# Performance work log

Hardware: AMD Instinct MI355X
Metric: run time of the kernel (lower is better)

## Reference

```python
import jax, jax.numpy as jnp
import numpy as np

ALPHA = 0.2  # LeakyReLU negative slope
N = 1024     # num_particles
DIM = 3
F_IN = 2 * DIM   # 6
NH = 64          # n_hidden_features
H = 4            # n_heads
T = 12


def _gat_attend(feat, a_vec, slope):
    # feat: (..., N, K); a_vec: (..., 2K) split into source/dest halves
    k = feat.shape[-1]
    f_src = jnp.einsum('...nk,...k->...n', feat, a_vec[..., :k])
    f_dst = jnp.einsum('...nk,...k->...n', feat, a_vec[..., k:])
    e = jax.nn.leaky_relu(f_src[..., :, None] + f_dst[..., None, :], slope)
    attn = jax.nn.softmax(e, axis=-1)  # (..., N, N) dense particle attention
    return jnp.einsum('...ij,...jk->...ik', attn, feat)


def pat_layer(x, W_heads, a_heads, W_out, a_out):
    # x: (N, F_IN); W_heads: (H, F_IN, NH); a_heads: (H, 2*NH)
    # W_out: (H*NH, F_OUT); a_out: (2*F_OUT)
    hW = jnp.einsum('nf,hfk->hnk', x, W_heads)          # (H, N, NH)
    heads = jax.nn.elu(_gat_attend(hW, a_heads, ALPHA))  # (H, N, NH)
    x2 = heads.transpose(1, 0, 2).reshape(x.shape[0], -1)  # (N, H*NH) concat
    hW2 = x2 @ W_out                                     # (N, F_OUT)
    return _gat_attend(hW2, a_out, ALPHA)                # output head, no elu


def setup_inputs() -> dict:
    key = jax.random.key(0)
    ks = jax.random.split(key, 13)
    s = 0.1
    d = {'states': jax.random.normal(ks[0], (T, N, F_IN), jnp.float32)}
    names = ['Wx', 'ax', 'Wxo', 'axo', 'Wh', 'ah', 'Who', 'aho', 'Wy', 'ay', 'Wyo', 'ayo']
    shapes = [(H, F_IN, NH), (H, 2 * NH), (H * NH, F_IN), (2 * F_IN)] * 3
    for i, (nm, sh) in enumerate(zip(names, shapes)):
        sh = sh if isinstance(sh, tuple) else (sh,)
        d[nm] = s * jax.random.normal(ks[i + 1], sh, jnp.float32)
    return d


def reference(states, Wx, ax, Wxo, axo, Wh, ah, Who, aho, Wy, ay, Wyo, ayo):
    def step(h_prev, x_t):
        h_t = pat_layer(x_t, Wx, ax, Wxo, axo) + pat_layer(h_prev, Wh, ah, Who, aho)
        y_t = x_t + pat_layer(h_t, Wy, ay, Wyo, ayo)
        return h_t, y_t

    h0 = jnp.zeros((N, F_IN), states.dtype)
    _, ys = jax.lax.scan(step, h0, states)
    return ys  # (T, N, 2*dim)
```

## Files before the change

### kernel.cpp

```cpp
#include <hip/hip_runtime.h>
#include <hip/hip_bf16.h>

#define ALPHA 0.2f

typedef float v2f __attribute__((ext_vector_type(2)));
typedef short bf16x8 __attribute__((ext_vector_type(8)));
typedef float f32x4 __attribute__((ext_vector_type(4)));

__device__ __forceinline__ float wsum(float v){
  #pragma unroll
  for (int m = 1; m < 64; m <<= 1) v += __shfl_xor(v, m, 64);
  return v;
}
__device__ __forceinline__ float wmax(float v){
  #pragma unroll
  for (int m = 1; m < 64; m <<= 1) v = fmaxf(v, __shfl_xor(v, m, 64));
  return v;
}

__global__ void k_detect(const unsigned short* __restrict__ s, int n, int* __restrict__ flag){
  int i = blockIdx.x * 256 + threadIdx.x;
  if (i < n){
    unsigned short u = s[i];
    if ((u & 0x7F80u) == 0x7F80u) atomicOr(flag, 1);
  }
}

struct Ptr13 { const void* p[13]; };
__global__ void k_cvtAll(Ptr13 src, float* __restrict__ xs, float* __restrict__ wsW,
                         const int* __restrict__ flag){
  const int n = blockIdx.x * 256 + threadIdx.x;
  const int F = *flag;
  if (n < 73728){
    xs[n] = F ? ((const float*)src.p[0])[n]
              : __bfloat162float(((const __hip_bfloat16*)src.p[0])[n]);
    return;
  }
  const int m = n - 73728;
  if (m >= 10788) return;
  const int segend[12] = {1536,2048,3584,3596,5132,5644,7180,7192,8728,9240,10776,10788};
  const int dstoff[12] = {0,1536,2048,3584,3600,5136,5648,7184,7200,8736,9248,10784};
  int seg = 0;
  #pragma unroll
  for (int i = 0; i < 12; ++i) if (m >= segend[i]) seg = i + 1;
  const int local = m - (seg ? segend[seg - 1] : 0);
  float v;
  if (F) v = ((const float*)src.p[seg + 1])[local];
  else   v = __bfloat162float(((const __hip_bfloat16*)src.p[seg + 1])[local]);
  wsW[dstoff[seg] + local] = v;
}

__launch_bounds__(256)
__global__ void k_prepT(const float* __restrict__ X, const float* __restrict__ W,
                        const float* __restrict__ a,
                        __hip_bfloat16* __restrict__ Vt, float* __restrict__ fsd)
{
  __shared__ float WS[384];
  __shared__ float aS[128];
  __shared__ __align__(16) __hip_bfloat16 tileT[64 * 264];
  const int t = threadIdx.x;
  const int b = blockIdx.y;
  const int h = blockIdx.z;
  const int row0 = blockIdx.x * 256;
  const int row = row0 + t;
  for (int i = t; i < 384; i += 256) WS[i] = W[h * 384 + i];
  if (t < 128) aS[t] = a[h * 128 + t];
  __syncthreads();
  float x[6];
  const float* xp = X + ((size_t)b * 1024 + row) * 6;
  #pragma unroll
  for (int f = 0; f < 6; ++f) x[f] = xp[f];
  float fs = 0.f, fd = 0.f;
  for (int k = 0; k < 64; ++k){
    float v = 0.f;
    #pragma unroll
    for (int f = 0; f < 6; ++f) v += x[f] * WS[f * 64 + k];
    fs += v * aS[k]; fd += v * aS[64 + k];
    tileT[k * 264 + t] = __float2bfloat16(v);
  }
  fsd[(((size_t)b * 4 + h) * 2 + 0) * 1024 + row] = fs;
  fsd[(((size_t)b * 4 + h) * 2 + 1) * 1024 + row] = fd;
  __syncthreads();
  const int k = t >> 2, seg = t & 3;
  __hip_bfloat16* dst = Vt + (((size_t)b * 4 + h) * 64 + k) * 1032 + row0 + seg * 64;
  const __hip_bfloat16* src = tileT + k * 264 + seg * 64;
  #pragma unroll
  for (int i = 0; i < 8; ++i)
    ((uint4*)dst)[i] = ((const uint4*)src)[i];
}

__launch_bounds__(256)
__global__ void k_attM(const __hip_bfloat16* __restrict__ Vt, const float* __restrict__ fsd,
                       const float* __restrict__ Wout, const float* __restrict__ aout,
                       float* __restrict__ hW2part, float* __restrict__ f2part)
{
  const int h = blockIdx.x & 3;
  const int row0 = (blockIdx.x >> 2) * 64;
  const int b = blockIdx.y;
  const int t = threadIdx.x;
  const int wv = t >> 6, lane = t & 63;
  const int n = lane & 15, q = lane >> 4;
  const size_t bh = (size_t)b * 4 + h;

  __shared__ float dS[1024];
  __shared__ __align__(16) __hip_bfloat16 VbS[64 * 72];
  __shared__ float WoS[384];
  __shared__ float aoS[12];
  __shared__ float redW[4];

  const __hip_bfloat16* Vbase = Vt + bh * 64 * 1032;
  const int sfeat = t >> 3, sc = (t & 7) * 8;
  const __hip_bfloat16* g0 = Vbase + (size_t)sfeat * 1032 + sc;
  const __hip_bfloat16* g1 = Vbase + (size_t)(sfeat + 32) * 1032 + sc;

  uint4 ra = *(const uint4*)(g0);
  uint4 rb = *(const uint4*)(g1);

  const float* fb = fsd + bh * 2048;
  float4 dv = *(const float4*)(fb + 1024 + t * 4);
  for (int i = t; i < 384; i += 256) WoS[i] = Wout[h * 384 + i];
  if (t < 12) aoS[t] = aout[t];
  *(float4*)&dS[t * 4] = dv;
  const float sW = fb[row0 + wv * 16 + n];
  float lm = fmaxf(fmaxf(dv.x, dv.y), fmaxf(dv.z, dv.w));
  lm = wmax(lm);
  if (lane == 0) redW[wv] = lm;
  __syncthreads();
  const float maxd = fmaxf(fmaxf(redW[0], redW[1]), fmaxf(redW[2], redW[3]));
  float mW = sW + maxd; mW = fmaxf(mW, ALPHA * mW);

  *(uint4*)&VbS[sfeat * 72 + sc] = ra;
  *(uint4*)&VbS[(sfeat + 32) * 72 + sc] = rb;
  __syncthreads();

  f32x4 acc[4];
  #pragma unroll
  for (int nt = 0; nt < 4; ++nt) acc[nt] = (f32x4){0.f, 0.f, 0.f, 0.f};
  float den = 0.f;

  for (int jt = 0; jt < 16; ++jt){
    uint4 r2a, r2b;
    if (jt < 15){
      r2a = *(const uint4*)(g0 + (jt + 1) * 64);
      r2b = *(const uint4*)(g1 + (jt + 1) * 64);
    }
    const float* dp = &dS[jt * 64 + q * 8];
    float d0[8], d1[8];
    *(float4*)&d0[0] = *(const float4*)(dp);
    *(float4*)&d0[4] = *(const float4*)(dp + 4);
    *(float4*)&d1[0] = *(const float4*)(dp + 32);
    *(float4*)&d1[4] = *(const float4*)(dp + 36);
    bf16x8 a0, a1;
    #pragma unroll
    for (int i = 0; i < 8; ++i){
      float e0 = sW + d0[i]; e0 = fmaxf(e0, ALPHA * e0);
      __hip_bfloat16 w0 = __float2bfloat16(__expf(fminf(e0 - mW, 0.f)));
      a0[i] = __builtin_bit_cast(short, w0);
      den += __bfloat162float(w0);
      float e1 = sW + d1[i]; e1 = fmaxf(e1, ALPHA * e1);
      __hip_bfloat16 w1 = __float2bfloat16(__expf(fminf(e1 - mW, 0.f)));
      a1[i] = __builtin_bit_cast(short, w1);
      den += __bfloat162float(w1);
    }
    const __hip_bfloat16* vb = &VbS[0];
    #pragma unroll
    for (int nt = 0; nt < 4; ++nt){
      bf16x8 b0 = *(const bf16x8*)(vb + (nt * 16 + n) * 72 + q * 8);
      acc[nt] = __builtin_amdgcn_mfma_f32_16x16x32_bf16(a0, b0, acc[nt], 0, 0, 0);
    }
    #pragma unroll
    for (int nt = 0; nt < 4; ++nt){
      bf16x8 b1 = *(const bf16x8*)(vb + (nt * 16 + n) * 72 + 32 + q * 8);
      acc[nt] = __builtin_amdgcn_mfma_f32_16x16x32_bf16(a1, b1, acc[nt], 0, 0, 0);
    }
    __syncthreads();
    if (jt < 15){
      *(uint4*)&VbS[sfeat * 72 + sc] = r2a;
      *(uint4*)&VbS[(sfeat + 32) * 72 + sc] = r2b;
    }
    __syncthreads();
  }
  den += __shfl_xor(den, 16, 64);
  den += __shfl_xor(den, 32, 64);

  float o[4][6];
  #pragma unroll
  for (int reg = 0; reg < 4; ++reg)
    #pragma unroll
    for (int f = 0; f < 6; ++f) o[reg][f] = 0.f;
  #pragma unroll
  for (int reg = 0; reg < 4; ++reg){
    const float dn = __shfl(den, q * 4 + reg, 64);
    #pragma unroll
    for (int nt = 0; nt < 4; ++nt){
      float v = acc[nt][reg] / dn;
      v = v > 0.f ? v : (__expf(v) - 1.f);
      #pragma unroll
      for (int f = 0; f < 6; ++f) o[reg][f] += v * WoS[(nt * 16 + n) * 6 + f];
    }
  }
  #pragma unroll
  for (int mm = 1; mm < 16; mm <<= 1)
    #pragma unroll
    for (int reg = 0; reg < 4; ++reg)
      #pragma unroll
      for (int f = 0; f < 6; ++f) o[reg][f] += __shfl_xor(o[reg][f], mm, 64);
  if (n == 0){
    #pragma unroll
    for (int reg = 0; reg < 4; ++reg){
      const int row = row0 + wv * 16 + q * 4 + reg;
      float* hp = hW2part + bh * 6144 + row * 6;
      float fs = 0.f, fd = 0.f;
      #pragma unroll
      for (int f = 0; f < 6; ++f){
        hp[f] = o[reg][f];
        fs += o[reg][f] * aoS[f]; fd += o[reg][f] * aoS[6 + f];
      }
      f2part[bh * 2048 + row]        = fs;
      f2part[bh * 2048 + 1024 + row] = fd;
    }
  }
}

template<int R>
__launch_bounds__(256)
__global__ void k_attA(const __hip_bfloat16* __restrict__ Vb, const float* __restrict__ fsd,
                       const float* __restrict__ Wout, const float* __restrict__ aout,
                       float* __restrict__ hW2part, float* __restrict__ f2part)
{
  const int h = blockIdx.x & 3;
  const int row0 = (blockIdx.x >> 2) * R;
  const int b = blockIdx.y;
  const int t = threadIdx.x;
  const int wv = t >> 6, lane = t & 63;
  const int kq = t & 15, sp = t >> 4;
  const int j0 = sp * 64;

  __shared__ float WoS[384];
  __shared__ float aoS[12];
  __shared__ float dS[1024];
  __shared__ float sS[R];
  __shared__ float wT[R * 1024 + 64];
  __shared__ float accS[4][R][64];
  __shared__ float denP[R][256 / R];
  __shared__ float redW[4];

  for (int i = t; i < 384; i += 256) WoS[i] = Wout[h * 384 + i];
  if (t < 12) aoS[t] = aout[t];
  const float* fbase = fsd + ((size_t)b * 4 + h) * 2048;
  for (int i = t; i < 1024; i += 256) dS[i] = fbase[1024 + i];
  if (t < R) sS[t] = fbase[row0 + t];
  __syncthreads();
  float lm = -1.0e30f;
  for (int i = t; i < 1024; i += 256) lm = fmaxf(lm, dS[i]);
  lm = wmax(lm);
  if (lane == 0) redW[wv] = lm;
  __syncthreads();
  const float maxd = fmaxf(fmaxf(redW[0], redW[1]), fmaxf(redW[2], redW[3]));
  {
    const int rW = t & (R - 1);
    const float sW = sS[rW];
    float smW = sW + maxd;
    const float mW = smW > 0.f ? smW : ALPHA * smW;
    float dpart = 0.f;
    for (int g = t; g < R * 1024; g += 256){
      const int jj = g / R;
      float e = sW + dS[jj]; e = e > 0.f ? e : ALPHA * e;
      float w = __expf(fminf(e - mW, 0.f));
      wT[jj * R + ((((jj >> 2) + (jj >> 6)) & 7) << 2) + rW] = w;
      dpart += w;
    }
    denP[rW][t / R] = dpart;
  }
  __syncthreads();
  const __hip_bfloat16* V = Vb + ((size_t)b * 4 + h) * 65536 + (size_t)j0 * 64 + kq * 4;
  v2f acc0[R], acc1[R];
  #pragma unroll
  for (int r = 0; r < R; ++r){ acc0[r] = (v2f)(0.f); acc1[r] = (v2f)(0.f); }
  for (int i = 0; i < 64; i += 2){
    uint2 u0 = *(const uint2*)(V + (size_t)i * 64);
    uint2 u1 = *(const uint2*)(V + (size_t)(i + 1) * 64);
    const int sw = ((sp * 17 + (i >> 2)) & 7) << 2;
    const float* w0p = &wT[(j0 + i) * R + sw];
    const float* w1p = w0p + R;
    float w0[R], w1[R];
    #pragma unroll
    for (int qq = 0; qq < R / 4; ++qq){
      *(float4*)&w0[4*qq] = *(const float4*)(w0p + 4*qq);
      *(float4*)&w1[4*qq] = *(const float4*)(w1p + 4*qq);
    }
    v2f v0a = {__uint_as_float(u0.x << 16), __uint_as_float(u0.x & 0xffff0000u)};
    v2f v0b = {__uint_as_float(u0.y << 16), __uint_as_float(u0.y & 0xffff0000u)};
    v2f v1a = {__uint_as_float(u1.x << 16), __uint_as_float(u1.x & 0xffff0000u)};
    v2f v1b = {__uint_as_float(u1.y << 16), __uint_as_float(u1.y & 0xffff0000u)};
    #pragma unroll
    for (int r = 0; r < R; ++r){
      v2f w0v = {w0[r], w0[r]};
      v2f w1v = {w1[r], w1[r]};
      acc0[r] += w0v * v0a;
      acc1[r] += w0v * v0b;
      acc0[r] += w1v * v1a;
      acc1[r] += w1v * v1b;
    }
  }
  #pragma unroll
  for (int r = 0; r < R; ++r){
    float a4[4] = {acc0[r].x, acc0[r].y, acc1[r].x, acc1[r].y};
    #pragma unroll
    for (int qq = 0; qq < 4; ++qq){
      a4[qq] += __shfl_xor(a4[qq], 16, 64);
      a4[qq] += __shfl_xor(a4[qq], 32, 64);
    }
    if (lane < 16){
      #pragma unroll
      for (int qq = 0; qq < 4; ++qq) accS[wv][r][kq * 4 + qq] = a4[qq];
    }
  }
  __syncthreads();
  #pragma unroll
  for (int i = 0; i < R / 4; ++i){
    const int r = wv + 4 * i, row = row0 + r;
    float vsum = accS[0][r][lane] + accS[1][r][lane]
               + accS[2][r][lane] + accS[3][r][lane];
    float dsum = 0.f;
    for (int s2 = 0; s2 < 256 / R; ++s2) dsum += denP[r][s2];
    float v = vsum / dsum;
    v = v > 0.f ? v : (__expf(v) - 1.f);
    float o[6];
    #pragma unroll
    for (int f = 0; f < 6; ++f) o[f] = wsum(v * WoS[lane * 6 + f]);
    if (lane == 0){
      float fs = 0.f, fd = 0.f;
      float* hp = hW2part + ((size_t)b * 4 + h) * 6144;
      #pragma unroll
      for (int f = 0; f < 6; ++f){
        hp[row * 6 + f] = o[f];
        fs += o[f] * aoS[f]; fd += o[f] * aoS[6 + f];
      }
      f2part[((size_t)b * 4 + h) * 2048 + row]        = fs;
      f2part[((size_t)b * 4 + h) * 2048 + 1024 + row] = fd;
    }
  }
}

__launch_bounds__(256)
__global__ void k_attB(const float* __restrict__ hW2part, const float* __restrict__ f2part,
                       const float* __restrict__ Lx_t, float* __restrict__ h_t,
                       const float* __restrict__ Wh, const float* __restrict__ ah,
                       __hip_bfloat16* __restrict__ hWn, float* __restrict__ fn)
{
  const int t = threadIdx.x;
  const int row0 = blockIdx.x * 4;
  const int wv = t >> 6, lane = t & 63;
  __shared__ float featS[6144];
  __shared__ float dS[1024];
  __shared__ float sS[4];
  __shared__ float redW[4];
  __shared__ float htS[4][6];
  __shared__ float WnS[1536];
  __shared__ float anS[512];

  for (int i = t; i < 6144; i += 256)
    featS[i] = hW2part[i] + hW2part[6144 + i] + hW2part[12288 + i] + hW2part[18432 + i];
  for (int i = t; i < 1024; i += 256)
    dS[i] = f2part[1024 + i] + f2part[3072 + i] + f2part[5120 + i] + f2part[7168 + i];
  if (t < 4){
    const int r = row0 + t;
    sS[t] = f2part[r] + f2part[2048 + r] + f2part[4096 + r] + f2part[6144 + r];
  }
  for (int i = t; i < 1536; i += 256) WnS[i] = Wh[i];
  for (int i = t; i < 512;  i += 256) anS[i] = ah[i];
  __syncthreads();
  float lm = -1.0e30f;
  for (int i = t; i < 1024; i += 256) lm = fmaxf(lm, dS[i]);
  lm = wmax(lm);
  if (lane == 0) redW[wv] = lm;
  __syncthreads();
  const float maxd = fmaxf(fmaxf(redW[0], redW[1]), fmaxf(redW[2], redW[3]));
  {
    const int r = wv, row = row0 + r;
    const float s = sS[r];
    float m = s + maxd; m = m > 0.f ? m : ALPHA * m;
    float num[6] = {0.f,0.f,0.f,0.f,0.f,0.f};
    float den = 0.f;
    for (int j = lane; j < 1024; j += 64){
      float e = s + dS[j]; e = e > 0.f ? e : ALPHA * e;
      float w = __expf(fminf(e - m, 0.f));
      den += w;
      const float* fr = &featS[j * 6];
      #pragma unroll
      for (int f = 0; f < 6; ++f) num[f] += w * fr[f];
    }
    den = wsum(den);
    #pragma unroll
    for (int f = 0; f < 6; ++f) num[f] = wsum(num[f]);
    if (lane == 0){
      #pragma unroll
      for (int f = 0; f < 6; ++f){
        float hv = Lx_t[row * 6 + f] + num[f] / den;
        h_t[row * 6 + f] = hv;
        htS[r][f] = hv;
      }
    }
  }
  __syncthreads();
  {
    const int k = lane, rw = row0 + wv;
    float hv[6];
    #pragma unroll
    for (int f = 0; f < 6; ++f) hv[f] = htS[wv][f];
    #pragma unroll
    for (int h = 0; h < 4; ++h){
      float acc = 0.f;
      #pragma unroll
      for (int f = 0; f < 6; ++f) acc += hv[f] * WnS[(h * 6 + f) * 64 + k];
      hWn[((size_t)h * 1024 + rw) * 64 + k] = __float2bfloat16(acc);
      float ps = wsum(acc * anS[h * 128 + k]);
      float pd = wsum(acc * anS[h * 128 + 64 + k]);
      if (k == 0){
        fn[((size_t)h * 2 + 0) * 1024 + rw] = ps;
        fn[((size_t)h * 2 + 1) * 1024 + rw] = pd;
      }
    }
  }
}

template<int MODE>
__launch_bounds__(256)
__global__ void k_attO(const float* __restrict__ hW2part, const float* __restrict__ f2part,
                       const float* __restrict__ addsrc, float* __restrict__ outf,
                       void* __restrict__ outv, int outOff, const int* __restrict__ flag)
{
  const int b = blockIdx.y;
  const int row0 = blockIdx.x * 16;
  const int t = threadIdx.x;
  const int wv = t >> 6, lane = t & 63;
  __shared__ float featS[6144];
  __shared__ float dS[1024];
  __shared__ float sS[16];
  __shared__ float redW[4];

  const float* hp = hW2part + (size_t)b * 24576;
  for (int i = t; i < 6144; i += 256)
    featS[i] = hp[i] + hp[6144 + i] + hp[12288 + i] + hp[18432 + i];
  const float* fp = f2part + (size_t)b * 8192;
  for (int i = t; i < 1024; i += 256)
    dS[i] = fp[1024 + i] + fp[3072 + i] + fp[5120 + i] + fp[7168 + i];
  if (t < 16){
    const int r = row0 + t;
    sS[t] = fp[r] + fp[2048 + r] + fp[4096 + r] + fp[6144 + r];
  }
  __syncthreads();
  float lm = -1.0e30f;
  for (int i = t; i < 1024; i += 256) lm = fmaxf(lm, dS[i]);
  lm = wmax(lm);
  if (lane == 0) redW[wv] = lm;
  __syncthreads();
  const float maxd = fmaxf(fmaxf(redW[0], redW[1]), fmaxf(redW[2], redW[3]));

  const int r = t >> 4, jq = t & 15;
  const int row = row0 + r;
  const float s = sS[r];
  float m = s + maxd; m = m > 0.f ? m : ALPHA * m;
  float num[6] = {0.f,0.f,0.f,0.f,0.f,0.f};
  float den = 0.f;
  for (int j = jq; j < 1024; j += 16){
    float e = s + dS[j]; e = e > 0.f ? e : ALPHA * e;
    float w = __expf(fminf(e - m, 0.f));
    den += w;
    const float* fr = &featS[j * 6];
    #pragma unroll
    for (int f = 0; f < 6; ++f) num[f] += w * fr[f];
  }
  #pragma unroll
  for (int mm = 1; mm < 16; mm <<= 1){
    den += __shfl_xor(den, mm, 64);
    #pragma unroll
    for (int f = 0; f < 6; ++f) num[f] += __shfl_xor(num[f], mm, 64);
  }

  if (jq == 0){
    if (MODE == 0){
      float* dst = outf + ((size_t)b * 1024 + row) * 6;
      #pragma unroll
      for (int f = 0; f < 6; ++f) dst[f] = num[f] / den;
    } else {
      const float* xsrc = addsrc + ((size_t)b * 1024 + row) * 6;
      const int base = outOff + b * 6144 + row * 6;
      if (*flag){
        float* dst = (float*)outv;
        #pragma unroll
        for (int f = 0; f < 6; ++f) dst[base + f] = xsrc[f] + num[f] / den;
      } else {
        __hip_bfloat16* dst = (__hip_bfloat16*)outv;
        #pragma unroll
        for (int f = 0; f < 6; ++f) dst[base + f] = __float2bfloat16(xsrc[f] + num[f] / den);
      }
    }
  }
}

extern "C" void kernel_launch(void* const* d_in, const int* in_sizes, int n_in,
                              void* d_out, int out_size, void* d_ws, size_t ws_size,
                              hipStream_t stream) {
  (void)in_sizes; (void)n_in; (void)out_size;

  const size_t avail = ws_size / 4;
  int CH = 0;
  const int cands[6] = {12, 6, 4, 3, 2, 1};
  for (int i = 0; i < 6; ++i){
    if (232000u + (size_t)cands[i] * 303104u <= avail){ CH = cands[i]; break; }
  }
  if (CH == 0) return;

  float* ws = (float*)d_ws;
  size_t off = 0;
  int*   flag = (int*)(ws + off); off += 16;
  float* xs   = ws + off; off += 73728;
  float* wsW  = ws + off; off += 10800;
  float* Lx    = ws + off; off += 73728;
  float* h_all = ws + off; off += 73728;
  float* p2hW2 = ws + off; off += (size_t)CH * 24576;
  float* p2f2  = ws + off; off += (size_t)CH * 8192;
  float* hWc   = ws + off; off += (size_t)CH * 262144;
  float* fc    = ws + off; off += (size_t)CH * 8192;

  hipMemsetAsync(flag, 0, 4, stream);
  k_detect<<<288, 256, 0, stream>>>((const unsigned short*)d_in[0], 73728, flag);
  Ptr13 ptrs;
  for (int i = 0; i < 13; ++i) ptrs.p[i] = d_in[i];
  k_cvtAll<<<331, 256, 0, stream>>>(ptrs, xs, wsW, flag);

  const int dstoff[12] = {0,1536,2048,3584,3600,5136,5648,7184,7200,8736,9248,10784};
  float *Wx = wsW + dstoff[0], *ax = wsW + dstoff[1], *Wxo = wsW + dstoff[2], *axo = wsW + dstoff[3];
  float *Wh = wsW + dstoff[4], *ah = wsW + dstoff[5], *Who = wsW + dstoff[6], *aho = wsW + dstoff[7];
  float *Wy = wsW + dstoff[8], *ay = wsW + dstoff[9], *Wyo = wsW + dstoff[10], *ayo = wsW + dstoff[11];

  __hip_bfloat16* VtG = (__hip_bfloat16*)hWc;

  for (int t0 = 0; t0 < 12; t0 += CH){
    k_prepT<<<dim3(4, CH, 4), 256, 0, stream>>>(xs + (size_t)t0 * 6144, Wx, ax, VtG, fc);
    k_attM<<<dim3(64, CH), 256, 0, stream>>>(VtG, fc, Wxo, axo, p2hW2, p2f2);
    k_attO<0><<<dim3(64, CH), 256, 0, stream>>>(p2hW2, p2f2, nullptr, Lx + (size_t)t0 * 6144,
                                                nullptr, 0, flag);
  }

  __hip_bfloat16* hWhB = (__hip_bfloat16*)hWc;
  float* fh = fc;
  hipMemsetAsync(hWhB, 0, 4 * 1024 * 64 * sizeof(__hip_bfloat16), stream);
  hipMemsetAsync(fh,  0, 8192 * sizeof(float), stream);
  for (int t = 0; t < 12; ++t){
    k_attA<4><<<dim3(1024, 1), 256, 0, stream>>>(hWhB, fh, Who, aho, p2hW2, p2f2);
    k_attB<<<256, 256, 0, stream>>>(p2hW2, p2f2, Lx + (size_t)t * 6144,
                                    h_all + (size_t)t * 6144, Wh, ah, hWhB, fh);
  }

  for (int t0 = 0; t0 < 12; t0 += CH){
    k_prepT<<<dim3(4, CH, 4), 256, 0, stream>>>(h_all + (size_t)t0 * 6144, Wy, ay, VtG, fc);
    k_attM<<<dim3(64, CH), 256, 0, stream>>>(VtG, fc, Wyo, ayo, p2hW2, p2f2);
    k_attO<2><<<dim3(64, CH), 256, 0, stream>>>(p2hW2, p2f2, xs + (size_t)t0 * 6144, nullptr,
                                                d_out, t0 * 6144, flag);
  }
}
```

Baseline: 514.6 us.

## Use MFMA in recurrent attention kernel and load V directly from global

Replaces the scalar FMA recurrent attention kernel (k_attA, 4 rows per block) with an MFMA-based k_attP that handles 16 rows per block and splits the key dimension across four waves, reducing partial sums through shared memory. k_attB now writes hW in a feature-major transposed layout so the MFMA B operands can be read straight from global. k_attM also drops its shared-memory double-buffering of V in favour of direct per-lane global loads, removing two barriers per iteration. The trade is fewer blocks and the loss of explicit prefetch, so the kernels lean on cache and latency hiding for the global reads.

Measured after the change: 417.5 us. 1.23x faster.

```diff
diff --git a/kernel.cpp b/kernel.cpp
--- a/kernel.cpp
+++ b/kernel.cpp
@@ -103,18 +103,9 @@
   const size_t bh = (size_t)b * 4 + h;
 
   __shared__ float dS[1024];
-  __shared__ __align__(16) __hip_bfloat16 VbS[64 * 72];
   __shared__ float WoS[384];
   __shared__ float aoS[12];
   __shared__ float redW[4];
-
-  const __hip_bfloat16* Vbase = Vt + bh * 64 * 1032;
-  const int sfeat = t >> 3, sc = (t & 7) * 8;
-  const __hip_bfloat16* g0 = Vbase + (size_t)sfeat * 1032 + sc;
-  const __hip_bfloat16* g1 = Vbase + (size_t)(sfeat + 32) * 1032 + sc;
-
-  uint4 ra = *(const uint4*)(g0);
-  uint4 rb = *(const uint4*)(g1);
 
   const float* fb = fsd + bh * 2048;
   float4 dv = *(const float4*)(fb + 1024 + t * 4);
@@ -129,20 +120,18 @@
   const float maxd = fmaxf(fmaxf(redW[0], redW[1]), fmaxf(redW[2], redW[3]));
   float mW = sW + maxd; mW = fmaxf(mW, ALPHA * mW);
 
-  *(uint4*)&VbS[sfeat * 72 + sc] = ra;
-  *(uint4*)&VbS[(sfeat + 32) * 72 + sc] = rb;
-  __syncthreads();
-
+  const __hip_bfloat16* vbase = Vt + (bh * 64 + n) * 1032 + q * 8;
   f32x4 acc[4];
   #pragma unroll
   for (int nt = 0; nt < 4; ++nt) acc[nt] = (f32x4){0.f, 0.f, 0.f, 0.f};
   float den = 0.f;
 
   for (int jt = 0; jt < 16; ++jt){
-    uint4 r2a, r2b;
-    if (jt < 15){
-      r2a = *(const uint4*)(g0 + (jt + 1) * 64);
-      r2b = *(const uint4*)(g1 + (jt + 1) * 64);
+    bf16x8 b0[4], b1[4];
+    #pragma unroll
+    for (int nt = 0; nt < 4; ++nt){
+      b0[nt] = *(const bf16x8*)(vbase + nt * 16512 + jt * 64);
+      b1[nt] = *(const bf16x8*)(vbase + nt * 16512 + jt * 64 + 32);
     }
     const float* dp = &dS[jt * 64 + q * 8];
     float d0[8], d1[8];
@@ -162,23 +151,12 @@
       a1[i] = __builtin_bit_cast(short, w1);
       den += __bfloat162float(w1);
     }
-    const __hip_bfloat16* vb = &VbS[0];
-    #pragma unroll
-    for (int nt = 0; nt < 4; ++nt){
-      bf16x8 b0 = *(const bf16x8*)(vb + (nt * 16 + n) * 72 + q * 8);
-      acc[nt] = __builtin_amdgcn_mfma_f32_16x16x32_bf16(a0, b0, acc[nt], 0, 0, 0);
-    }
-    #pragma unroll
-    for (int nt = 0; nt < 4; ++nt){
-      bf16x8 b1 = *(const bf16x8*)(vb + (nt * 16 + n) * 72 + 32 + q * 8);
-      acc[nt] = __builtin_amdgcn_mfma_f32_16x16x32_bf16(a1, b1, acc[nt], 0, 0, 0);
-    }
-    __syncthreads();
-    if (jt < 15){
-      *(uint4*)&VbS[sfeat * 72 + sc] = r2a;
-      *(uint4*)&VbS[(sfeat + 32) * 72 + sc] = r2b;
-    }
-    __syncthreads();
+    #pragma unroll
+    for (int nt = 0; nt < 4; ++nt)
+      acc[nt] = __builtin_amdgcn_mfma_f32_16x16x32_bf16(a0, b0[nt], acc[nt], 0, 0, 0);
+    #pragma unroll
+    for (int nt = 0; nt < 4; ++nt)
+      acc[nt] = __builtin_amdgcn_mfma_f32_16x16x32_bf16(a1, b1[nt], acc[nt], 0, 0, 0);
   }
   den += __shfl_xor(den, 16, 64);
   den += __shfl_xor(den, 32, 64);
@@ -222,124 +200,113 @@
   }
 }
 
-template<int R>
 __launch_bounds__(256)
-__global__ void k_attA(const __hip_bfloat16* __restrict__ Vb, const float* __restrict__ fsd,
+__global__ void k_attP(const __hip_bfloat16* __restrict__ VtP, const float* __restrict__ fsd,
                        const float* __restrict__ Wout, const float* __restrict__ aout,
                        float* __restrict__ hW2part, float* __restrict__ f2part)
 {
   const int h = blockIdx.x & 3;
-  const int row0 = (blockIdx.x >> 2) * R;
-  const int b = blockIdx.y;
+  const int row0 = (blockIdx.x >> 2) * 16;
   const int t = threadIdx.x;
   const int wv = t >> 6, lane = t & 63;
-  const int kq = t & 15, sp = t >> 4;
-  const int j0 = sp * 64;
-
+  const int n = lane & 15, q = lane >> 4;
+
+  __shared__ float dS[1024];
   __shared__ float WoS[384];
   __shared__ float aoS[12];
-  __shared__ float dS[1024];
-  __shared__ float sS[R];
-  __shared__ float wT[R * 1024 + 64];
-  __shared__ float accS[4][R][64];
-  __shared__ float denP[R][256 / R];
   __shared__ float redW[4];
-
+  __shared__ float accS[4][16][65];
+  __shared__ float denP[4][16];
+
+  const float* fb = fsd + (size_t)h * 2048;
+  float4 dv = *(const float4*)(fb + 1024 + t * 4);
   for (int i = t; i < 384; i += 256) WoS[i] = Wout[h * 384 + i];
   if (t < 12) aoS[t] = aout[t];
-  const float* fbase = fsd + ((size_t)b * 4 + h) * 2048;
-  for (int i = t; i < 1024; i += 256) dS[i] = fbase[1024 + i];
-  if (t < R) sS[t] = fbase[row0 + t];
-  __syncthreads();
-  float lm = -1.0e30f;
-  for (int i = t; i < 1024; i += 256) lm = fmaxf(lm, dS[i]);
+  *(float4*)&dS[t * 4] = dv;
+  const float sW = fb[row0 + n];
+  float lm = fmaxf(fmaxf(dv.x, dv.y), fmaxf(dv.z, dv.w));
   lm = wmax(lm);
   if (lane == 0) redW[wv] = lm;
   __syncthreads();
   const float maxd = fmaxf(fmaxf(redW[0], redW[1]), fmaxf(redW[2], redW[3]));
-  {
-    const int rW = t & (R - 1);
-    const float sW = sS[rW];
-    float smW = sW + maxd;
-    const float mW = smW > 0.f ? smW : ALPHA * smW;
-    float dpart = 0.f;
-    for (int g = t; g < R * 1024; g += 256){
-      const int jj = g / R;
-      float e = sW + dS[jj]; e = e > 0.f ? e : ALPHA * e;
-      float w = __expf(fminf(e - mW, 0.f));
-      wT[jj * R + ((((jj >> 2) + (jj >> 6)) & 7) << 2) + rW] = w;
-      dpart += w;
-    }
-    denP[rW][t / R] = dpart;
-  }
-  __syncthreads();
-  const __hip_bfloat16* V = Vb + ((size_t)b * 4 + h) * 65536 + (size_t)j0 * 64 + kq * 4;
-  v2f acc0[R], acc1[R];
-  #pragma unroll
-  for (int r = 0; r < R; ++r){ acc0[r] = (v2f)(0.f); acc1[r] = (v2f)(0.f); }
-  for (int i = 0; i < 64; i += 2){
-    uint2 u0 = *(const uint2*)(V + (size_t)i * 64);
-    uint2 u1 = *(const uint2*)(V + (size_t)(i + 1) * 64);
-    const int sw = ((sp * 17 + (i >> 2)) & 7) << 2;
-    const float* w0p = &wT[(j0 + i) * R + sw];
-    const float* w1p = w0p + R;
-    float w0[R], w1[R];
-    #pragma unroll
-    for (int qq = 0; qq < R / 4; ++qq){
-      *(float4*)&w0[4*qq] = *(const float4*)(w0p + 4*qq);
-      *(float4*)&w1[4*qq] = *(const float4*)(w1p + 4*qq);
-    }
-    v2f v0a = {__uint_as_float(u0.x << 16), __uint_as_float(u0.x & 0xffff0000u)};
-    v2f v0b = {__uint_as_float(u0.y << 16), __uint_as_float(u0.y & 0xffff0000u)};
-    v2f v1a = {__uint_as_float(u1.x << 16), __uint_as_float(u1.x & 0xffff0000u)};
-    v2f v1b = {__uint_as_float(u1.y << 16), __uint_as_float(u1.y & 0xffff0000u)};
-    #pragma unroll
-    for (int r = 0; r < R; ++r){
-      v2f w0v = {w0[r], w0[r]};
-      v2f w1v = {w1[r], w1[r]};
-      acc0[r] += w0v * v0a;
-      acc1[r] += w0v * v0b;
-      acc0[r] += w1v * v1a;
-      acc1[r] += w1v * v1b;
-    }
-  }
-  #pragma unroll
-  for (int r = 0; r < R; ++r){
-    float a4[4] = {acc0[r].x, acc0[r].y, acc1[r].x, acc1[r].y};
-    #pragma unroll
-    for (int qq = 0; qq < 4; ++qq){
-      a4[qq] += __shfl_xor(a4[qq], 16, 64);
-      a4[qq] += __shfl_xor(a4[qq], 32, 64);
-    }
-    if (lane < 16){
-      #pragma unroll
-      for (int qq = 0; qq < 4; ++qq) accS[wv][r][kq * 4 + qq] = a4[qq];
-    }
-  }
-  __syncthreads();
-  #pragma unroll
-  for (int i = 0; i < R / 4; ++i){
-    const int r = wv + 4 * i, row = row0 + r;
-    float vsum = accS[0][r][lane] + accS[1][r][lane]
-               + accS[2][r][lane] + accS[3][r][lane];
-    float dsum = 0.f;
-    for (int s2 = 0; s2 < 256 / R; ++s2) dsum += denP[r][s2];
-    float v = vsum / dsum;
+  float mW = sW + maxd; mW = fmaxf(mW, ALPHA * mW);
+
+  const __hip_bfloat16* vbase = VtP + ((size_t)h * 64 + n) * 1024 + q * 8;
+  f32x4 acc[4];
+  #pragma unroll
+  for (int nt = 0; nt < 4; ++nt) acc[nt] = (f32x4){0.f, 0.f, 0.f, 0.f};
+  float den = 0.f;
+
+  #pragma unroll
+  for (int u = 0; u < 4; ++u){
+    const int jt = wv * 4 + u;
+    bf16x8 b0[4], b1[4];
+    #pragma unroll
+    for (int nt = 0; nt < 4; ++nt){
+      b0[nt] = *(const bf16x8*)(vbase + nt * 16384 + jt * 64);
+      b1[nt] = *(const bf16x8*)(vbase + nt * 16384 + jt * 64 + 32);
+    }
+    const float* dp = &dS[jt * 64 + q * 8];
+    float d0[8], d1[8];
+    *(float4*)&d0[0] = *(const float4*)(dp);
+    *(float4*)&d0[4] = *(const float4*)(dp + 4);
+    *(float4*)&d1[0] = *(const float4*)(dp + 32);
+    *(float4*)&d1[4] = *(const float4*)(dp + 36);
+    bf16x8 a0, a1;
+    #pragma unroll
+    for (int i = 0; i < 8; ++i){
+      float e0 = sW + d0[i]; e0 = fmaxf(e0, ALPHA * e0);
+      __hip_bfloat16 w0 = __float2bfloat16(__expf(fminf(e0 - mW, 0.f)));
+      a0[i] = __builtin_bit_cast(short, w0);
+      den += __bfloat162float(w0);
+      float e1 = sW + d1[i]; e1 = fmaxf(e1, ALPHA * e1);
+      __hip_bfloat16 w1 = __float2bfloat16(__expf(fminf(e1 - mW, 0.f)));
+      a1[i] = __builtin_bit_cast(short, w1);
+      den += __bfloat162float(w1);
+    }
+    #pragma unroll
+    for (int nt = 0; nt < 4; ++nt)
+      acc[nt] = __builtin_amdgcn_mfma_f32_16x16x32_bf16(a0, b0[nt], acc[nt], 0, 0, 0);
+    #pragma unroll
+    for (int nt = 0; nt < 4; ++nt)
+      acc[nt] = __builtin_amdgcn_mfma_f32_16x16x32_bf16(a1, b1[nt], acc[nt], 0, 0, 0);
+  }
+  den += __shfl_xor(den, 16, 64);
+  den += __shfl_xor(den, 32, 64);
+  if (lane < 16) denP[wv][lane] = den;
+  #pragma unroll
+  for (int nt = 0; nt < 4; ++nt)
+    #pragma unroll
+    for (int reg = 0; reg < 4; ++reg)
+      accS[wv][q * 4 + reg][nt * 16 + n] = acc[nt][reg];
+  __syncthreads();
+
+  const int r = t >> 4, kq = t & 15;
+  const float dn = denP[0][r] + denP[1][r] + denP[2][r] + denP[3][r];
+  float o[6] = {0.f,0.f,0.f,0.f,0.f,0.f};
+  #pragma unroll
+  for (int j4 = 0; j4 < 4; ++j4){
+    const int k = kq * 4 + j4;
+    float v = (accS[0][r][k] + accS[1][r][k] + accS[2][r][k] + accS[3][r][k]) / dn;
     v = v > 0.f ? v : (__expf(v) - 1.f);
-    float o[6];
-    #pragma unroll
-    for (int f = 0; f < 6; ++f) o[f] = wsum(v * WoS[lane * 6 + f]);
-    if (lane == 0){
-      float fs = 0.f, fd = 0.f;
-      float* hp = hW2part + ((size_t)b * 4 + h) * 6144;
-      #pragma unroll
-      for (int f = 0; f < 6; ++f){
-        hp[row * 6 + f] = o[f];
-        fs += o[f] * aoS[f]; fd += o[f] * aoS[6 + f];
-      }
-      f2part[((size_t)b * 4 + h) * 2048 + row]        = fs;
-      f2part[((size_t)b * 4 + h) * 2048 + 1024 + row] = fd;
-    }
+    #pragma unroll
+    for (int f = 0; f < 6; ++f) o[f] += v * WoS[k * 6 + f];
+  }
+  #pragma unroll
+  for (int mm = 1; mm < 16; mm <<= 1)
+    #pragma unroll
+    for (int f = 0; f < 6; ++f) o[f] += __shfl_xor(o[f], mm, 64);
+  if (kq == 0){
+    const int row = row0 + r;
+    float* hp = hW2part + (size_t)h * 6144 + row * 6;
+    float fs = 0.f, fd = 0.f;
+    #pragma unroll
+    for (int f = 0; f < 6; ++f){
+      hp[f] = o[f];
+      fs += o[f] * aoS[f]; fd += o[f] * aoS[6 + f];
+    }
+    f2part[(size_t)h * 2048 + row]        = fs;
+    f2part[(size_t)h * 2048 + 1024 + row] = fd;
   }
 }
 
@@ -414,7 +381,7 @@
       float acc = 0.f;
       #pragma unroll
       for (int f = 0; f < 6; ++f) acc += hv[f] * WnS[(h * 6 + f) * 64 + k];
-      hWn[((size_t)h * 1024 + rw) * 64 + k] = __float2bfloat16(acc);
+      hWn[((size_t)h * 64 + k) * 1024 + rw] = __float2bfloat16(acc);
       float ps = wsum(acc * anS[h * 128 + k]);
       float pd = wsum(acc * anS[h * 128 + 64 + k]);
       if (k == 0){
@@ -545,14 +512,14 @@
                                                 nullptr, 0, flag);
   }
 
-  __hip_bfloat16* hWhB = (__hip_bfloat16*)hWc;
+  __hip_bfloat16* VtP = (__hip_bfloat16*)hWc;
   float* fh = fc;
-  hipMemsetAsync(hWhB, 0, 4 * 1024 * 64 * sizeof(__hip_bfloat16), stream);
+  hipMemsetAsync(VtP, 0, 4 * 64 * 1024 * sizeof(__hip_bfloat16), stream);
   hipMemsetAsync(fh,  0, 8192 * sizeof(float), stream);
   for (int t = 0; t < 12; ++t){
-    k_attA<4><<<dim3(1024, 1), 256, 0, stream>>>(hWhB, fh, Who, aho, p2hW2, p2f2);
+    k_attP<<<dim3(256, 1), 256, 0, stream>>>(VtP, fh, Who, aho, p2hW2, p2f2);
     k_attB<<<256, 256, 0, stream>>>(p2hW2, p2f2, Lx + (size_t)t * 6144,
-                                    h_all + (size_t)t * 6144, Wh, ah, hWhB, fh);
+                                    h_all + (size_t)t * 6144, Wh, ah, VtP, fh);
   }
 
   for (int t0 = 0; t0 < 12; t0 += CH){
```
